# Performance work log

Hardware: AMD Instinct MI355X
Metric: run time of the kernel (lower is better)

The kernel has to match this reference:

```python
import jax, jax.numpy as jnp
import numpy as np

EPS = float(np.finfo(np.float32).eps)  # torch.finfo(float32).eps


def _inv2x2(M):
    """Elementwise inverse of 2x2 complex matrices. M: (..., 2, 2) complex."""
    det = M[..., 0, 0] * M[..., 1, 1] - M[..., 0, 1] * M[..., 1, 0]
    # matches torch _inv: conj(z) / |z|^2
    inv_det = jnp.conj(det) / (jnp.abs(det) ** 2)
    row0 = jnp.stack([inv_det * M[..., 1, 1], -inv_det * M[..., 0, 1]], axis=-1)
    row1 = jnp.stack([-inv_det * M[..., 1, 0], inv_det * M[..., 0, 0]], axis=-1)
    return jnp.stack([row0, row1], axis=-2)


def _em(y, x, iterations):
    # y: (F, B, C, 2, S) real/imag; x: (F, B, C, 2)
    yc = y[..., 0, :] + 1j * y[..., 1, :]          # (F, B, C, S) complex
    xc = x[..., 0] + 1j * x[..., 1]                # (F, B, C)   complex
    nb_channels = yc.shape[2]
    reg = jnp.sqrt(jnp.asarray(EPS, jnp.float32)) * jnp.eye(
        nb_channels, dtype=yc.dtype)               # sqrt(eps)*I regularizer
    v = jnp.mean(jnp.abs(yc) ** 2, axis=2)         # (F, B, S)
    R = jnp.einsum('fbcs,fbds->bcds', yc, jnp.conj(yc))
    for _ in range(iterations):
        # E-step: PSD = channel-average power spectrogram
        v = jnp.mean(jnp.abs(yc) ** 2, axis=2)     # (F, B, S)
        # spatial covariance: sum_f y y^H / (eps + sum_f v)  -> (B, C, C, S)
        R = jnp.einsum('fbcs,fbds->bcds', yc, jnp.conj(yc))
        R = R / (EPS + jnp.sum(v, axis=0))[:, None, None, :]
        # mixture covariance Cxx = sqrt(eps)*I + sum_j v_j R_j  -> (F, B, C, C)
        Cxx = reg[None, None] + jnp.einsum('fbs,bcds->fbcd', v, R)
        inv_Cxx = _inv2x2(Cxx)
        # Wiener gain G_j = v_j * R_j @ inv_Cxx  -> (F, B, C, C, S)
        gain = jnp.einsum('fbs,bcks,fbkd->fbcds', v, R, inv_Cxx)
        # apply filter: y_j = G_j @ x
        yc = jnp.einsum('fbcds,fbd->fbcs', gain, xc)
    y_out = jnp.stack([jnp.real(yc), jnp.imag(yc)], axis=-2)   # (F, B, C, 2, S)
    R_out = jnp.stack([jnp.real(R), jnp.imag(R)], axis=-2)     # (B, C, C, 2, S)
    return y_out, v, R_out


def setup_inputs() -> dict:
    key = jax.random.key(0)
    k1, k2 = jax.random.split(key)
    F, B, C, S = 1000, 2049, 2, 4
    y = jax.random.normal(k1, (F, B, C, 2, S), dtype=jnp.float32)
    x = jax.random.normal(k2, (F, B, C, 2), dtype=jnp.float32)
    return {"y": y, "x": x, "iterations": 2}


def reference(y, x, iterations):
    return _em(y, x, iterations)
```

## Files before the change

### kernel.cpp

```cpp
#include <hip/hip_runtime.h>

#define FDIM 1000
#define BDIM 2049
#define NTH  256
#define FS   8
#define FT   125
#define BT   16
#define NBT  129
#define GRID (NBT * FS)

#define V_OFF 32784000ull
#define R_OFF 40980000ull

#define P2_OFF ((size_t)BDIM * FS * 20)

#define EPSF 1.1920928955078125e-07f
#define REGC 3.4526698300124393e-04f

__device__ __forceinline__ float4 shflx4(float4 v, int m) {
    float4 r;
    r.x = __shfl_xor(v.x, m);
    r.y = __shfl_xor(v.y, m);
    r.z = __shfl_xor(v.z, m);
    r.w = __shfl_xor(v.w, m);
    return r;
}

__device__ __forceinline__ void xpose4(float4& r0, float4& r1, float4& r2, float4& r3,
                                       int lane) {
    const bool c0 = (lane & 16) != 0;
    const bool c1 = (lane & 32) != 0;
    {
        float4 a  = c0 ? r0 : r1;
        float4 bb = shflx4(a, 16);
        if (c0) r0 = bb; else r1 = bb;
        float4 a2 = c0 ? r2 : r3;
        float4 b2 = shflx4(a2, 16);
        if (c0) r2 = b2; else r3 = b2;
    }
    {
        float4 a  = c1 ? r0 : r2;
        float4 bb = shflx4(a, 32);
        if (c1) r0 = bb; else r2 = bb;
        float4 a2 = c1 ? r1 : r3;
        float4 b2 = shflx4(a2, 32);
        if (c1) r1 = b2; else r3 = b2;
    }
}

__global__ __launch_bounds__(NTH) void k1_power(
    const float* __restrict__ y, float* __restrict__ v, float* __restrict__ part1)
{
    const int btile = blockIdx.x / FS;
    const int fs    = blockIdx.x % FS;
    const int tid   = threadIdx.x;
    const int lane  = tid & 63;
    const int p     = lane & 15;
    const int cq    = lane >> 4;
    const int w     = tid >> 6;
    const int b     = btile * BT + p;
    const bool vb   = (b < BDIM);
    const int f0    = fs * FT;

    const float4* __restrict__ y4 = reinterpret_cast<const float4*>(y);
    float4* __restrict__ v4 = reinterpret_cast<float4*>(v);

    float acc[20];
    #pragma unroll
    for (int j = 0; j < 20; ++j) acc[j] = 0.f;

    #pragma unroll
    for (int ii = 0; ii < 8; ++ii) {
        const int fob = ii * 16 + 4 * w;
        float4 q0 = make_float4(0.f,0.f,0.f,0.f), q1 = q0, q2 = q0, q3 = q0;
        if (vb) {
            if (fob + 0 < FT) q0 = y4[((size_t)(f0+fob+0)*BDIM + b)*4 + cq];
            if (fob + 1 < FT) q1 = y4[((size_t)(f0+fob+1)*BDIM + b)*4 + cq];
            if (fob + 2 < FT) q2 = y4[((size_t)(f0+fob+2)*BDIM + b)*4 + cq];
            if (fob + 3 < FT) q3 = y4[((size_t)(f0+fob+3)*BDIM + b)*4 + cq];
        }
        xpose4(q0, q1, q2, q3, lane);
        const int fo = fob + cq;
        if (fo < FT && vb) {
            const size_t e = (size_t)(f0 + fo) * BDIM + b;
            const float y0r[4] = {q0.x,q0.y,q0.z,q0.w};
            const float y0i[4] = {q1.x,q1.y,q1.z,q1.w};
            const float y1r[4] = {q2.x,q2.y,q2.z,q2.w};
            const float y1i[4] = {q3.x,q3.y,q3.z,q3.w};
            float vv[4];
            #pragma unroll
            for (int s = 0; s < 4; ++s) {
                const float p0 = y0r[s]*y0r[s] + y0i[s]*y0i[s];
                const float p1 = y1r[s]*y1r[s] + y1i[s]*y1i[s];
                vv[s] = 0.5f * (p0 + p1);
                acc[s]    += p0;
                acc[4+s]  += p1;
                acc[8+s]  += y0r[s]*y1r[s] + y0i[s]*y1i[s];
                acc[12+s] += y0i[s]*y1r[s] - y0r[s]*y1i[s];
                acc[16+s] += vv[s];
            }
            v4[e] = make_float4(vv[0], vv[1], vv[2], vv[3]);
        }
    }
    #pragma unroll
    for (int j = 0; j < 20; ++j) {
        float t = acc[j];
        t += __shfl_xor(t, 16);
        t += __shfl_xor(t, 32);
        acc[j] = t;
    }
    __shared__ float red[4][16][20];
    if ((tid & 63) < 16) {
        #pragma unroll
        for (int j = 0; j < 20; ++j) red[w][p][j] = acc[j];
    }
    __syncthreads();
    for (int idx = tid; idx < 320; idx += NTH) {
        const int bss = idx & 15, j = idx >> 4;
        const int bb = btile * BT + bss;
        if (bb < BDIM)
            part1[((size_t)bb * FS + fs) * 20 + j] =
                red[0][bss][j] + red[1][bss][j] + red[2][bss][j] + red[3][bss][j];
    }
}

__global__ __launch_bounds__(NTH) void k3_em(
    const float* __restrict__ x, float* __restrict__ v,
    const float* __restrict__ part1, float* __restrict__ part2,
    const int* __restrict__ itp)
{
    const int btile = blockIdx.x / FS;
    const int fs    = blockIdx.x % FS;
    const int tid   = threadIdx.x;
    const int bs    = tid & 15;
    const int fi    = tid >> 4;
    const int wid   = tid >> 6;
    const int b     = btile * BT + bs;
    const bool vb   = (b < BDIM);
    const int iters = itp[0];

    __shared__ float rsumS[16][20];
    __shared__ float rnormS[16][16];
    for (int idx = tid; idx < 320; idx += NTH) {
        const int bss = idx & 15, j = idx >> 4;
        const int bb = btile * BT + bss;
        float s = 0.f;
        if (bb < BDIM) {
            #pragma unroll
            for (int q = 0; q < FS; ++q) s += part1[((size_t)bb * FS + q) * 20 + j];
        }
        rsumS[bss][j] = s;
    }
    __syncthreads();
    {
        const int bss = tid & 15, j = tid >> 4;
        rnormS[bss][j] = rsumS[bss][j] / (EPSF + rsumS[bss][16 + (j & 3)]);
    }
    __syncthreads();

    if (iters <= 1) {
        for (int idx = tid; idx < 320; idx += NTH) {
            const int bss = idx & 15, j = idx >> 4;
            const int bb = btile * BT + bss;
            if (bb < BDIM)
                part2[((size_t)bb * FS + fs) * 20 + j] = (fs == 0) ? rsumS[bss][j] : 0.f;
        }
        return;
    }

    float rn00[4], rn11[4], rn01r[4], rn01i[4];
    #pragma unroll
    for (int s = 0; s < 4; ++s) {
        rn00[s]=rnormS[bs][s]; rn11[s]=rnormS[bs][4+s];
        rn01r[s]=rnormS[bs][8+s]; rn01i[s]=rnormS[bs][12+s];
    }

    float acc[20];
    #pragma unroll
    for (int j = 0; j < 20; ++j) acc[j] = 0.f;

    const int f0 = fs * FT;
    #pragma unroll
    for (int ii = 0; ii < 8; ++ii) {
        const int fo = ii * 16 + fi;
        if (fo < FT && vb) {
            const int f = f0 + fo;
            const size_t e = (size_t)f * BDIM + b;
            float4 vv4 = reinterpret_cast<const float4*>(v)[e];
            float4 xv  = reinterpret_cast<const float4*>(x)[e];
            float v1[4] = {vv4.x, vv4.y, vv4.z, vv4.w};
            float c00 = REGC, c11 = REGC, c01r = 0.f, c01i = 0.f;
            #pragma unroll
            for (int s = 0; s < 4; ++s) {
                c00  += v1[s]*rn00[s];
                c11  += v1[s]*rn11[s];
                c01r += v1[s]*rn01r[s];
                c01i += v1[s]*rn01i[s];
            }
            const float det  = c00*c11 - (c01r*c01r + c01i*c01i);
            const float invd = det / (det*det);
            const float i00 = invd*c11, i11 = invd*c00;
            const float i01r = -invd*c01r, i01i = -invd*c01i;
            const float xr0 = xv.x, xi0 = xv.y, xr1 = xv.z, xi1 = xv.w;
            const float w0r = i00*xr0 + (i01r*xr1 - i01i*xi1);
            const float w0i = i00*xi0 + (i01r*xi1 + i01i*xr1);
            const float w1r = (i01r*xr0 + i01i*xi0) + i11*xr1;
            const float w1i = (i01r*xi0 - i01i*xr0) + i11*xi1;
            float v2[4];
            #pragma unroll
            for (int s = 0; s < 4; ++s) {
                const float vs = v1[s];
                const float y0r = vs*(rn00[s]*w0r + (rn01r[s]*w1r - rn01i[s]*w1i));
                const float y0i = vs*(rn00[s]*w0i + (rn01r[s]*w1i + rn01i[s]*w1r));
                const float y1r = vs*((rn01r[s]*w0r + rn01i[s]*w0i) + rn11[s]*w1r);
                const float y1i = vs*((rn01r[s]*w0i - rn01i[s]*w0r) + rn11[s]*w1i);
                const float p0 = y0r*y0r + y0i*y0i;
                const float p1 = y1r*y1r + y1i*y1i;
                v2[s] = 0.5f*(p0 + p1);
                acc[s]    += p0;
                acc[4+s]  += p1;
                acc[8+s]  += y0r*y1r + y0i*y1i;
                acc[12+s] += y0i*y1r - y0r*y1i;
                acc[16+s] += v2[s];
            }
            reinterpret_cast<float4*>(v)[e] = make_float4(v2[0], v2[1], v2[2], v2[3]);
        }
    }
    #pragma unroll
    for (int j = 0; j < 20; ++j) {
        float t = acc[j];
        t += __shfl_xor(t, 16);
        t += __shfl_xor(t, 32);
        acc[j] = t;
    }
    __shared__ float red[4][16][20];
    if ((tid & 63) < 16) {
        #pragma unroll
        for (int j = 0; j < 20; ++j) red[wid][bs][j] = acc[j];
    }
    __syncthreads();
    for (int idx = tid; idx < 320; idx += NTH) {
        const int bss = idx & 15, j = idx >> 4;
        const int bb = btile * BT + bss;
        if (bb < BDIM)
            part2[((size_t)bb * FS + fs) * 20 + j] =
                red[0][bss][j] + red[1][bss][j] + red[2][bss][j] + red[3][bss][j];
    }
}

__global__ __launch_bounds__(NTH) void k5_final(
    const float* __restrict__ y, const float* __restrict__ x, const float* __restrict__ v,
    const float* __restrict__ part2, float* __restrict__ yout, float* __restrict__ Rout,
    const int* __restrict__ itp)
{
    const int btile = blockIdx.x / FS;
    const int fs    = blockIdx.x % FS;
    const int tid   = threadIdx.x;
    const int lane  = tid & 63;
    const int p     = lane & 15;
    const int cq    = lane >> 4;
    const int w     = tid >> 6;
    const int b     = btile * BT + p;
    const bool vb   = (b < BDIM);
    const int iters = itp[0];
    const int f0    = fs * FT;

    __shared__ float rsumS[16][20];
    __shared__ float rnormS[16][16];
    for (int idx = tid; idx < 320; idx += NTH) {
        const int bss = idx & 15, j = idx >> 4;
        const int bb = btile * BT + bss;
        float s = 0.f;
        if (bb < BDIM) {
            #pragma unroll
            for (int q = 0; q < FS; ++q) s += part2[((size_t)bb * FS + q) * 20 + j];
        }
        rsumS[bss][j] = s;
    }
    __syncthreads();
    {
        const int bss = tid & 15, j = tid >> 4;
        rnormS[bss][j] = rsumS[bss][j] / (EPSF + rsumS[bss][16 + (j & 3)]);
    }
    __syncthreads();

    if (fs == 0) {
        for (int idx = tid; idx < 512; idx += NTH) {
            const int bss = idx >> 5, r = idx & 31;
            const int bb = btile * BT + bss;
            if (bb < BDIM) {
                const int c = (r>>4)&1, d = (r>>3)&1, ri = (r>>2)&1, s = r&3;
                const bool raw = (iters == 0);
                float val;
                if (c == d) {
                    val = ri ? 0.f : (raw ? rsumS[bss][(c?4:0)+s] : rnormS[bss][(c?4:0)+s]);
                } else {
                    const float re = raw ? rsumS[bss][8+s]  : rnormS[bss][8+s];
                    const float im = raw ? rsumS[bss][12+s] : rnormS[bss][12+s];
                    val = ri ? (c == 0 ? im : -im) : re;
                }
                Rout[(size_t)bb * 32 + r] = val;
            }
        }
    }

    const float4* __restrict__ y4 = reinterpret_cast<const float4*>(y);
    const float4* __restrict__ v4 = reinterpret_cast<const float4*>(v);
    const float4* __restrict__ x4 = reinterpret_cast<const float4*>(x);
    float4* __restrict__ o4 = reinterpret_cast<float4*>(yout);

    if (iters == 0) {
        #pragma unroll
        for (int ii = 0; ii < 8; ++ii) {
            const int fob = ii * 16 + 4 * w;
            if (vb) {
                if (fob + 0 < FT) { const size_t i0 = ((size_t)(f0+fob+0)*BDIM + b)*4 + cq; o4[i0] = y4[i0]; }
                if (fob + 1 < FT) { const size_t i1 = ((size_t)(f0+fob+1)*BDIM + b)*4 + cq; o4[i1] = y4[i1]; }
                if (fob + 2 < FT) { const size_t i2 = ((size_t)(f0+fob+2)*BDIM + b)*4 + cq; o4[i2] = y4[i2]; }
                if (fob + 3 < FT) { const size_t i3 = ((size_t)(f0+fob+3)*BDIM + b)*4 + cq; o4[i3] = y4[i3]; }
            }
        }
        return;
    }

    float rn00[4], rn11[4], rn01r[4], rn01i[4];
    #pragma unroll
    for (int s = 0; s < 4; ++s) {
        rn00[s]=rnormS[p][s]; rn11[s]=rnormS[p][4+s];
        rn01r[s]=rnormS[p][8+s]; rn01i[s]=rnormS[p][12+s];
    }

    #pragma unroll
    for (int ii = 0; ii < 8; ++ii) {
        const int fob = ii * 16 + 4 * w;
        const int fo  = fob + cq;
        float4 q0 = make_float4(0.f,0.f,0.f,0.f), q1 = q0, q2 = q0, q3 = q0;
        if (fo < FT && vb) {
            const size_t e = (size_t)(f0 + fo) * BDIM + b;
            float4 vv4 = v4[e];
            float4 xv  = x4[e];
            float vcur[4] = {vv4.x, vv4.y, vv4.z, vv4.w};
            float c00 = REGC, c11 = REGC, c01r = 0.f, c01i = 0.f;
            #pragma unroll
            for (int s = 0; s < 4; ++s) {
                c00  += vcur[s]*rn00[s];
                c11  += vcur[s]*rn11[s];
                c01r += vcur[s]*rn01r[s];
                c01i += vcur[s]*rn01i[s];
            }
            const float det  = c00*c11 - (c01r*c01r + c01i*c01i);
            const float invd = det / (det*det);
            const float i00 = invd*c11, i11 = invd*c00;
            const float i01r = -invd*c01r, i01i = -invd*c01i;
            const float xr0 = xv.x, xi0 = xv.y, xr1 = xv.z, xi1 = xv.w;
            const float w0r = i00*xr0 + (i01r*xr1 - i01i*xi1);
            const float w0i = i00*xi0 + (i01r*xi1 + i01i*xr1);
            const float w1r = (i01r*xr0 + i01i*xi0) + i11*xr1;
            const float w1i = (i01r*xi0 - i01i*xr0) + i11*xi1;
            float o0r[4], o0i[4], o1r[4], o1i[4];
            #pragma unroll
            for (int s = 0; s < 4; ++s) {
                const float vs = vcur[s];
                o0r[s] = vs*(rn00[s]*w0r + (rn01r[s]*w1r - rn01i[s]*w1i));
                o0i[s] = vs*(rn00[s]*w0i + (rn01r[s]*w1i + rn01i[s]*w1r));
                o1r[s] = vs*((rn01r[s]*w0r + rn01i[s]*w0i) + rn11[s]*w1r);
                o1i[s] = vs*((rn01r[s]*w0i - rn01i[s]*w0r) + rn11[s]*w1i);
            }
            q0 = make_float4(o0r[0], o0r[1], o0r[2], o0r[3]);
            q1 = make_float4(o0i[0], o0i[1], o0i[2], o0i[3]);
            q2 = make_float4(o1r[0], o1r[1], o1r[2], o1r[3]);
            q3 = make_float4(o1i[0], o1i[1], o1i[2], o1i[3]);
        }
        xpose4(q0, q1, q2, q3, lane);
        if (vb) {
            if (fob + 0 < FT) o4[((size_t)(f0+fob+0)*BDIM + b)*4 + cq] = q0;
            if (fob + 1 < FT) o4[((size_t)(f0+fob+1)*BDIM + b)*4 + cq] = q1;
            if (fob + 2 < FT) o4[((size_t)(f0+fob+2)*BDIM + b)*4 + cq] = q2;
            if (fob + 3 < FT) o4[((size_t)(f0+fob+3)*BDIM + b)*4 + cq] = q3;
        }
    }
}

extern "C" void kernel_launch(void* const* d_in, const int* in_sizes, int n_in,
                              void* d_out, int out_size, void* d_ws, size_t ws_size,
                              hipStream_t stream) {
    const float* y   = (const float*)d_in[0];
    const float* x   = (const float*)d_in[1];
    const int*   itp = (const int*)d_in[2];
    float* out   = (float*)d_out;
    float* vreg  = out + V_OFF;
    float* Rreg  = out + R_OFF;
    float* part1 = (float*)d_ws;
    float* part2 = part1 + P2_OFF;

    k1_power<<<GRID, NTH, 0, stream>>>(y, vreg, part1);
    k3_em   <<<GRID, NTH, 0, stream>>>(x, vreg, part1, part2, itp);
    k5_final<<<GRID, NTH, 0, stream>>>(y, x, vreg, part2, out, Rreg, itp);
}
```

Before: 324.1 us.

## Double frequency split, reduce partials with atomics, reorder block index mapping

The frequency axis is split into 16 chunks of 63 instead of 8 chunks of 125, which doubles the grid and halves the per-block loop, and a per-chunk limit handles the shorter last chunk. Per-chunk partial sums are now combined with float atomicAdd into one buffer that a memset clears first, replacing the per-chunk slots that consumers summed by hand. Block indices now walk bin tiles fastest within each frequency chunk. This aims for better occupancy and less reduction traffic, at the cost of an extra memset launch, atomic contention, and a summation order that is no longer deterministic.

Result: no change. 327.1 us (+0.9%).

```diff
diff --git a/kernel.cpp b/kernel.cpp
--- a/kernel.cpp
+++ b/kernel.cpp
@@ -3,8 +3,8 @@
 #define FDIM 1000
 #define BDIM 2049
 #define NTH  256
-#define FS   8
-#define FT   125
+#define FS   16
+#define FT   63
 #define BT   16
 #define NBT  129
 #define GRID (NBT * FS)
@@ -12,7 +12,7 @@
 #define V_OFF 32784000ull
 #define R_OFF 40980000ull
 
-#define P2_OFF ((size_t)BDIM * FS * 20)
+#define PSZ   ((size_t)BDIM * 20)
 
 #define EPSF 1.1920928955078125e-07f
 #define REGC 3.4526698300124393e-04f
@@ -51,8 +51,8 @@
 __global__ __launch_bounds__(NTH) void k1_power(
     const float* __restrict__ y, float* __restrict__ v, float* __restrict__ part1)
 {
-    const int btile = blockIdx.x / FS;
-    const int fs    = blockIdx.x % FS;
+    const int fs    = blockIdx.x / NBT;
+    const int btile = blockIdx.x % NBT;
     const int tid   = threadIdx.x;
     const int lane  = tid & 63;
     const int p     = lane & 15;
@@ -61,6 +61,7 @@
     const int b     = btile * BT + p;
     const bool vb   = (b < BDIM);
     const int f0    = fs * FT;
+    const int flim  = (FDIM - f0 < FT) ? (FDIM - f0) : FT;
 
     const float4* __restrict__ y4 = reinterpret_cast<const float4*>(y);
     float4* __restrict__ v4 = reinterpret_cast<float4*>(v);
@@ -70,18 +71,18 @@
     for (int j = 0; j < 20; ++j) acc[j] = 0.f;
 
     #pragma unroll
-    for (int ii = 0; ii < 8; ++ii) {
+    for (int ii = 0; ii < 4; ++ii) {
         const int fob = ii * 16 + 4 * w;
         float4 q0 = make_float4(0.f,0.f,0.f,0.f), q1 = q0, q2 = q0, q3 = q0;
         if (vb) {
-            if (fob + 0 < FT) q0 = y4[((size_t)(f0+fob+0)*BDIM + b)*4 + cq];
-            if (fob + 1 < FT) q1 = y4[((size_t)(f0+fob+1)*BDIM + b)*4 + cq];
-            if (fob + 2 < FT) q2 = y4[((size_t)(f0+fob+2)*BDIM + b)*4 + cq];
-            if (fob + 3 < FT) q3 = y4[((size_t)(f0+fob+3)*BDIM + b)*4 + cq];
+            if (fob + 0 < flim) q0 = y4[((size_t)(f0+fob+0)*BDIM + b)*4 + cq];
+            if (fob + 1 < flim) q1 = y4[((size_t)(f0+fob+1)*BDIM + b)*4 + cq];
+            if (fob + 2 < flim) q2 = y4[((size_t)(f0+fob+2)*BDIM + b)*4 + cq];
+            if (fob + 3 < flim) q3 = y4[((size_t)(f0+fob+3)*BDIM + b)*4 + cq];
         }
         xpose4(q0, q1, q2, q3, lane);
         const int fo = fob + cq;
-        if (fo < FT && vb) {
+        if (fo < flim && vb) {
             const size_t e = (size_t)(f0 + fo) * BDIM + b;
             const float y0r[4] = {q0.x,q0.y,q0.z,q0.w};
             const float y0i[4] = {q1.x,q1.y,q1.z,q1.w};
@@ -119,8 +120,8 @@
         const int bss = idx & 15, j = idx >> 4;
         const int bb = btile * BT + bss;
         if (bb < BDIM)
-            part1[((size_t)bb * FS + fs) * 20 + j] =
-                red[0][bss][j] + red[1][bss][j] + red[2][bss][j] + red[3][bss][j];
+            atomicAdd(&part1[(size_t)bb * 20 + j],
+                red[0][bss][j] + red[1][bss][j] + red[2][bss][j] + red[3][bss][j]);
     }
 }
 
@@ -129,8 +130,8 @@
     const float* __restrict__ part1, float* __restrict__ part2,
     const int* __restrict__ itp)
 {
-    const int btile = blockIdx.x / FS;
-    const int fs    = blockIdx.x % FS;
+    const int fs    = blockIdx.x / NBT;
+    const int btile = blockIdx.x % NBT;
     const int tid   = threadIdx.x;
     const int bs    = tid & 15;
     const int fi    = tid >> 4;
@@ -138,18 +139,15 @@
     const int b     = btile * BT + bs;
     const bool vb   = (b < BDIM);
     const int iters = itp[0];
+    const int f0    = fs * FT;
+    const int flim  = (FDIM - f0 < FT) ? (FDIM - f0) : FT;
 
     __shared__ float rsumS[16][20];
     __shared__ float rnormS[16][16];
     for (int idx = tid; idx < 320; idx += NTH) {
         const int bss = idx & 15, j = idx >> 4;
         const int bb = btile * BT + bss;
-        float s = 0.f;
-        if (bb < BDIM) {
-            #pragma unroll
-            for (int q = 0; q < FS; ++q) s += part1[((size_t)bb * FS + q) * 20 + j];
-        }
-        rsumS[bss][j] = s;
+        rsumS[bss][j] = (bb < BDIM) ? part1[(size_t)bb * 20 + j] : 0.f;
     }
     __syncthreads();
     {
@@ -159,11 +157,13 @@
     __syncthreads();
 
     if (iters <= 1) {
-        for (int idx = tid; idx < 320; idx += NTH) {
-            const int bss = idx & 15, j = idx >> 4;
-            const int bb = btile * BT + bss;
-            if (bb < BDIM)
-                part2[((size_t)bb * FS + fs) * 20 + j] = (fs == 0) ? rsumS[bss][j] : 0.f;
+        if (fs == 0) {
+            for (int idx = tid; idx < 320; idx += NTH) {
+                const int bss = idx & 15, j = idx >> 4;
+                const int bb = btile * BT + bss;
+                if (bb < BDIM)
+                    part2[(size_t)bb * 20 + j] = rsumS[bss][j];
+            }
         }
         return;
     }
@@ -179,11 +179,10 @@
     #pragma unroll
     for (int j = 0; j < 20; ++j) acc[j] = 0.f;
 
-    const int f0 = fs * FT;
-    #pragma unroll
-    for (int ii = 0; ii < 8; ++ii) {
+    #pragma unroll
+    for (int ii = 0; ii < 4; ++ii) {
         const int fo = ii * 16 + fi;
-        if (fo < FT && vb) {
+        if (fo < flim && vb) {
             const int f = f0 + fo;
             const size_t e = (size_t)f * BDIM + b;
             float4 vv4 = reinterpret_cast<const float4*>(v)[e];
@@ -243,8 +242,8 @@
         const int bss = idx & 15, j = idx >> 4;
         const int bb = btile * BT + bss;
         if (bb < BDIM)
-            part2[((size_t)bb * FS + fs) * 20 + j] =
-                red[0][bss][j] + red[1][bss][j] + red[2][bss][j] + red[3][bss][j];
+            atomicAdd(&part2[(size_t)bb * 20 + j],
+                red[0][bss][j] + red[1][bss][j] + red[2][bss][j] + red[3][bss][j]);
     }
 }
 
@@ -253,8 +252,8 @@
     const float* __restrict__ part2, float* __restrict__ yout, float* __restrict__ Rout,
     const int* __restrict__ itp)
 {
-    const int btile = blockIdx.x / FS;
-    const int fs    = blockIdx.x % FS;
+    const int fs    = blockIdx.x / NBT;
+    const int btile = blockIdx.x % NBT;
     const int tid   = threadIdx.x;
     const int lane  = tid & 63;
     const int p     = lane & 15;
@@ -264,18 +263,14 @@
     const bool vb   = (b < BDIM);
     const int iters = itp[0];
     const int f0    = fs * FT;
+    const int flim  = (FDIM - f0 < FT) ? (FDIM - f0) : FT;
 
     __shared__ float rsumS[16][20];
     __shared__ float rnormS[16][16];
     for (int idx = tid; idx < 320; idx += NTH) {
         const int bss = idx & 15, j = idx >> 4;
         const int bb = btile * BT + bss;
-        float s = 0.f;
-        if (bb < BDIM) {
-            #pragma unroll
-            for (int q = 0; q < FS; ++q) s += part2[((size_t)bb * FS + q) * 20 + j];
-        }
-        rsumS[bss][j] = s;
+        rsumS[bss][j] = (bb < BDIM) ? part2[(size_t)bb * 20 + j] : 0.f;
     }
     __syncthreads();
     {
@@ -311,13 +306,13 @@
 
     if (iters == 0) {
         #pragma unroll
-        for (int ii = 0; ii < 8; ++ii) {
+        for (int ii = 0; ii < 4; ++ii) {
             const int fob = ii * 16 + 4 * w;
             if (vb) {
-                if (fob + 0 < FT) { const size_t i0 = ((size_t)(f0+fob+0)*BDIM + b)*4 + cq; o4[i0] = y4[i0]; }
-                if (fob + 1 < FT) { const size_t i1 = ((size_t)(f0+fob+1)*BDIM + b)*4 + cq; o4[i1] = y4[i1]; }
-                if (fob + 2 < FT) { const size_t i2 = ((size_t)(f0+fob+2)*BDIM + b)*4 + cq; o4[i2] = y4[i2]; }
-                if (fob + 3 < FT) { const size_t i3 = ((size_t)(f0+fob+3)*BDIM + b)*4 + cq; o4[i3] = y4[i3]; }
+                if (fob + 0 < flim) { const size_t i0 = ((size_t)(f0+fob+0)*BDIM + b)*4 + cq; o4[i0] = y4[i0]; }
+                if (fob + 1 < flim) { const size_t i1 = ((size_t)(f0+fob+1)*BDIM + b)*4 + cq; o4[i1] = y4[i1]; }
+                if (fob + 2 < flim) { const size_t i2 = ((size_t)(f0+fob+2)*BDIM + b)*4 + cq; o4[i2] = y4[i2]; }
+                if (fob + 3 < flim) { const size_t i3 = ((size_t)(f0+fob+3)*BDIM + b)*4 + cq; o4[i3] = y4[i3]; }
             }
         }
         return;
@@ -331,11 +326,11 @@
     }
 
     #pragma unroll
-    for (int ii = 0; ii < 8; ++ii) {
+    for (int ii = 0; ii < 4; ++ii) {
         const int fob = ii * 16 + 4 * w;
         const int fo  = fob + cq;
         float4 q0 = make_float4(0.f,0.f,0.f,0.f), q1 = q0, q2 = q0, q3 = q0;
-        if (fo < FT && vb) {
+        if (fo < flim && vb) {
             const size_t e = (size_t)(f0 + fo) * BDIM + b;
             float4 vv4 = v4[e];
             float4 xv  = x4[e];
@@ -373,10 +368,10 @@
         }
         xpose4(q0, q1, q2, q3, lane);
         if (vb) {
-            if (fob + 0 < FT) o4[((size_t)(f0+fob+0)*BDIM + b)*4 + cq] = q0;
-            if (fob + 1 < FT) o4[((size_t)(f0+fob+1)*BDIM + b)*4 + cq] = q1;
-            if (fob + 2 < FT) o4[((size_t)(f0+fob+2)*BDIM + b)*4 + cq] = q2;
-            if (fob + 3 < FT) o4[((size_t)(f0+fob+3)*BDIM + b)*4 + cq] = q3;
+            if (fob + 0 < flim) o4[((size_t)(f0+fob+0)*BDIM + b)*4 + cq] = q0;
+            if (fob + 1 < flim) o4[((size_t)(f0+fob+1)*BDIM + b)*4 + cq] = q1;
+            if (fob + 2 < flim) o4[((size_t)(f0+fob+2)*BDIM + b)*4 + cq] = q2;
+            if (fob + 3 < flim) o4[((size_t)(f0+fob+3)*BDIM + b)*4 + cq] = q3;
         }
     }
 }
@@ -391,8 +386,9 @@
     float* vreg  = out + V_OFF;
     float* Rreg  = out + R_OFF;
     float* part1 = (float*)d_ws;
-    float* part2 = part1 + P2_OFF;
-
+    float* part2 = part1 + PSZ;
+
+    hipMemsetAsync(part1, 0, 2 * PSZ * sizeof(float), stream);
     k1_power<<<GRID, NTH, 0, stream>>>(y, vreg, part1);
     k3_em   <<<GRID, NTH, 0, stream>>>(x, vreg, part1, part2, itp);
     k5_final<<<GRID, NTH, 0, stream>>>(y, x, vreg, part2, out, Rreg, itp);
```
